# Performance work log

Measured on AMD Instinct MI355X. Metric: run time of the kernel, lower is better.

The kernel has to match this reference:

```python
import jax, jax.numpy as jnp
import numpy as np

# Matches MMD_loss(bandwidths=[1,2,5,10,20])
BANDWIDTHS = np.array([1.0, 2.0, 5.0, 10.0, 20.0], dtype=np.float64)
GAMMAS = (1.0 / (2.0 * BANDWIDTHS ** 2)).astype(np.float32)  # per original forward

N1, N2, D = 4096, 4096, 256


def setup_inputs() -> dict:
    key = jax.random.key(0)
    k1, k2 = jax.random.split(key)
    x1 = jax.random.normal(k1, (N1, D), dtype=jnp.float32)
    x2 = jax.random.normal(k2, (N2, D), dtype=jnp.float32)
    return {"x1": x1, "x2": x2}


def _sqdist(a, b):
    # ||a_i - b_j||^2 via GEMM identity; computed ONCE instead of per-bandwidth.
    an = jnp.sum(a * a, axis=1)  # [Na]
    bn = jnp.sum(b * b, axis=1)  # [Nb]
    d = an[:, None] + bn[None, :] - 2.0 * (a @ b.T)  # [Na, Nb]
    return jnp.maximum(d, 0.0)


def reference(x1, x2):
    d1 = x1.shape[1]
    d2 = x2.shape[1]
    s1 = jnp.float32(np.sqrt(d1))
    s2 = jnp.float32(np.sqrt(d2))

    D11 = _sqdist(x1, x1)  # [N1, N1]
    D22 = _sqdist(x2, x2)  # [N2, N2]
    D12 = _sqdist(x1, x2)  # [N1, N2]

    nb = jnp.float32(len(GAMMAS))
    m11 = jnp.float32(0.0)
    m22 = jnp.float32(0.0)
    m12 = jnp.float32(0.0)
    # small fixed loop over bandwidths; fused exp + mean per bandwidth
    for g in GAMMAS:
        g = jnp.float32(g)
        m11 = m11 + jnp.mean(jnp.exp(-(s1 * g) * D11))
        m22 = m22 + jnp.mean(jnp.exp(-(s2 * g) * D22))
        m12 = m12 + jnp.mean(jnp.exp(-(s1 * g) * D12))  # original uses d1 here too
    m11, m22, m12 = m11 / nb, m22 / nb, m12 / nb
    return jnp.sqrt(m11 - 2.0 * m12 + m22)
```

## Files before the change

kernel.cpp:

```cpp
#include <hip/hip_runtime.h>
#include <stdint.h>

typedef __attribute__((ext_vector_type(8))) short short8;
typedef __attribute__((ext_vector_type(4))) float f32x4;

#define N_ROWS 4096
#define D_DIM  256
#define NT     8192
#define TILE   128
#define NTILE  64

__device__ __forceinline__ unsigned short f2bf(float f) {
  unsigned int u = __float_as_uint(f);
  u += 0x7fffu + ((u >> 16) & 1u);
  return (unsigned short)(u >> 16);
}

__device__ __forceinline__ void gload_lds16(const void* g, void* l) {
  __builtin_amdgcn_global_load_lds(
      (const __attribute__((address_space(1))) unsigned int*)g,
      (__attribute__((address_space(3))) unsigned int*)l, 16, 0, 0);
}

__global__ __launch_bounds__(256) void mmd_prep(
    const float* __restrict__ x1, const float* __restrict__ x2,
    unsigned short* __restrict__ Zb, float* __restrict__ norms) {
  const int t = threadIdx.x, w = t >> 6, l = t & 63;
  const int r = blockIdx.x * 4 + w;
  const float* src = (r < N_ROWS) ? (x1 + (size_t)r * D_DIM)
                                  : (x2 + (size_t)(r - N_ROWS) * D_DIM);
  const float4 v = *(const float4*)(src + l * 4);
  float sq = v.x * v.x + v.y * v.y + v.z * v.z + v.w * v.w;
#pragma unroll
  for (int off = 32; off > 0; off >>= 1) sq += __shfl_down(sq, off);
  if (l == 0) norms[r] = sq;
  ushort4 o;
  o.x = f2bf(v.x); o.y = f2bf(v.y); o.z = f2bf(v.z); o.w = f2bf(v.w);
  *(ushort4*)(Zb + (size_t)r * D_DIM + l * 4) = o;
}

__global__ __launch_bounds__(256) void mmd_main(
    const unsigned short* __restrict__ Zb,
    const float* __restrict__ norms,
    float* __restrict__ partials) {
  const int br = blockIdx.x, bc = blockIdx.y;
  const int pidx = br * NTILE + bc;
  const int t = threadIdx.x;
  if (bc > br) { if (t == 0) partials[pidx] = 0.0f; return; }

  __shared__ __align__(16) unsigned short As[TILE][32];
  __shared__ __align__(16) unsigned short Bs[TILE][32];
  __shared__ float nrow[TILE], ncol[TILE];
  __shared__ float red[256];

  const int w = t >> 6, l = t & 63;
  if (t < TILE) nrow[t] = norms[br * TILE + t];
  else          ncol[t - TILE] = norms[bc * TILE + (t - TILE)];

  const int wr = (w >> 1) * 64, wc = (w & 1) * 64;
  const int fr = l & 15, fq = l >> 4;

  f32x4 acc[4][4];
#pragma unroll
  for (int m = 0; m < 4; ++m)
#pragma unroll
    for (int n = 0; n < 4; ++n)
      acc[m][n] = (f32x4){0.0f, 0.0f, 0.0f, 0.0f};

  for (int k0 = 0; k0 < D_DIM; k0 += 32) {
#pragma unroll
    for (int q = 0; q < 2; ++q) {
      const int obase = w * 2048 + q * 1024;
      const int o = obase + l * 16;
      const int row = o >> 6;
      const int chunk = (o >> 4) & 3;
      const unsigned short* ga =
          Zb + (size_t)(br * TILE + row) * D_DIM + k0 + chunk * 8;
      const unsigned short* gb =
          Zb + (size_t)(bc * TILE + row) * D_DIM + k0 + chunk * 8;
      gload_lds16(ga, (char*)(&As[0][0]) + obase);
      gload_lds16(gb, (char*)(&Bs[0][0]) + obase);
    }
    __syncthreads();

    short8 a[4], b[4];
#pragma unroll
    for (int m = 0; m < 4; ++m)
      a[m] = *(const short8*)(&As[wr + m * 16 + fr][fq * 8]);
#pragma unroll
    for (int n = 0; n < 4; ++n)
      b[n] = *(const short8*)(&Bs[wc + n * 16 + fr][fq * 8]);
#pragma unroll
    for (int m = 0; m < 4; ++m)
#pragma unroll
      for (int n = 0; n < 4; ++n)
        acc[m][n] = __builtin_amdgcn_mfma_f32_16x16x32_bf16(a[m], b[n],
                                                            acc[m][n], 0, 0, 0);
    __syncthreads();
  }

  float factor = ((br < 32) == (bc < 32)) ? 1.0f : -1.0f;
  if (br != bc) factor *= 2.0f;
  const bool diag = (br == bc);

  float sum = 0.0f;
#pragma unroll
  for (int m = 0; m < 4; ++m) {
#pragma unroll
    for (int n = 0; n < 4; ++n) {
#pragma unroll
      for (int r = 0; r < 4; ++r) {
        const int i = wr + m * 16 + fq * 4 + r;
        const int j = wc + n * 16 + fr;
        float d = nrow[i] + ncol[j] - 2.0f * acc[m][n][r];
        d = fmaxf(d, 0.0f);
        const float u = __expf(-0.02f * d);
        const float u2 = u * u, u4 = u2 * u2;
        const float u8 = u4 * u4, u16 = u8 * u8;
        const float u32v = u16 * u16, u64v = u32v * u32v;
        const float u100 = u64v * u32v * u4;
        const float u200 = u100 * u100, u400 = u200 * u200;
        float S = u + u4 + u16 + u100 + u400;
        if (diag && i == j) S = 0.0f;
        sum += S;
      }
    }
  }
  sum *= factor;

  red[t] = sum;
  __syncthreads();
#pragma unroll
  for (int k = 128; k > 0; k >>= 1) {
    if (t < k) red[t] += red[t + k];
    __syncthreads();
  }
  if (t == 0) partials[pidx] = red[0];
}

__global__ __launch_bounds__(256) void mmd_finish(
    const float* __restrict__ partials, float* __restrict__ out) {
  __shared__ float red[256];
  const int t = threadIdx.x;
  float s = 0.0f;
  for (int i = t; i < NTILE * NTILE; i += 256) s += partials[i];
  red[t] = s;
  __syncthreads();
#pragma unroll
  for (int k = 128; k > 0; k >>= 1) {
    if (t < k) red[t] += red[t + k];
    __syncthreads();
  }
  if (t == 0) {
    const float total = red[0] + 40960.0f;
    out[0] = sqrtf(fmaxf(total, 0.0f) / 83886080.0f);
  }
}

extern "C" void kernel_launch(void* const* d_in, const int* in_sizes, int n_in,
                              void* d_out, int out_size, void* d_ws, size_t ws_size,
                              hipStream_t stream) {
  const float* x1 = (const float*)d_in[0];
  const float* x2 = (const float*)d_in[1];
  unsigned short* Zb = (unsigned short*)d_ws;
  float* norms = (float*)((char*)d_ws + (size_t)NT * D_DIM * 2);
  float* partials = norms + NT;
  float* out = (float*)d_out;

  mmd_prep<<<dim3(NT / 4), dim3(256), 0, stream>>>(x1, x2, Zb, norms);
  mmd_main<<<dim3(NTILE, NTILE), dim3(256), 0, stream>>>(Zb, norms, partials);
  mmd_finish<<<dim3(1), dim3(256), 0, stream>>>(partials, out);
}
```

Before: 61.29 us.

## Double-buffer K=64 tiles with swizzled LDS, triangular grid, fuse final reduction

The main kernel now launches only the lower-triangular tile blocks instead of a full 64x64 grid with early exits. The K loop uses 64-wide chunks held in double-buffered LDS, with an XOR swizzle to avoid bank conflicts, so the next chunk is prefetched while the current one computes. Norms are loaded straight into registers rather than staged through shared memory. The separate finish kernel is removed: the last block to finish, found through an atomic counter reset in the prep kernel, does the final reduction. This saves a launch and removes idle blocks, at the cost of more LDS per block (about 65KB) and possibly lower occupancy.

```diff
diff --git a/kernel.cpp b/kernel.cpp
--- a/kernel.cpp
+++ b/kernel.cpp
@@ -8,7 +8,9 @@
 #define D_DIM  256
 #define NT     8192
 #define TILE   128
+#define BK     64
 #define NTILE  64
+#define NBLK   (NTILE * (NTILE + 1) / 2)
 
 __device__ __forceinline__ unsigned short f2bf(float f) {
   unsigned int u = __float_as_uint(f);
@@ -24,7 +26,9 @@
 
 __global__ __launch_bounds__(256) void mmd_prep(
     const float* __restrict__ x1, const float* __restrict__ x2,
-    unsigned short* __restrict__ Zb, float* __restrict__ norms) {
+    unsigned short* __restrict__ Zb, float* __restrict__ norms,
+    unsigned int* __restrict__ counter) {
+  if (blockIdx.x == 0 && threadIdx.x == 0) *counter = 0u;
   const int t = threadIdx.x, w = t >> 6, l = t & 63;
   const int r = blockIdx.x * 4 + w;
   const float* src = (r < N_ROWS) ? (x1 + (size_t)r * D_DIM)
@@ -39,27 +43,43 @@
   *(ushort4*)(Zb + (size_t)r * D_DIM + l * 4) = o;
 }
 
-__global__ __launch_bounds__(256) void mmd_main(
+__global__ __launch_bounds__(256, 2) void mmd_main(
     const unsigned short* __restrict__ Zb,
     const float* __restrict__ norms,
-    float* __restrict__ partials) {
-  const int br = blockIdx.x, bc = blockIdx.y;
-  const int pidx = br * NTILE + bc;
+    float* partials, unsigned int* counter, float* out) {
+  __shared__ __align__(16) unsigned short As[2][TILE * BK];
+  __shared__ __align__(16) unsigned short Bs[2][TILE * BK];
+  __shared__ float red[256];
+  __shared__ int amLastSh;
+
+  const int p = blockIdx.x;
+  int br = (int)((sqrtf(8.0f * (float)p + 1.0f) - 1.0f) * 0.5f);
+  while ((br + 1) * (br + 2) / 2 <= p) ++br;
+  while (br * (br + 1) / 2 > p) --br;
+  const int bc = p - br * (br + 1) / 2;
+
   const int t = threadIdx.x;
-  if (bc > br) { if (t == 0) partials[pidx] = 0.0f; return; }
-
-  __shared__ __align__(16) unsigned short As[TILE][32];
-  __shared__ __align__(16) unsigned short Bs[TILE][32];
-  __shared__ float nrow[TILE], ncol[TILE];
-  __shared__ float red[256];
-
   const int w = t >> 6, l = t & 63;
-  if (t < TILE) nrow[t] = norms[br * TILE + t];
-  else          ncol[t - TILE] = norms[bc * TILE + (t - TILE)];
-
   const int wr = (w >> 1) * 64, wc = (w & 1) * 64;
   const int fr = l & 15, fq = l >> 4;
 
+  const int aRow0 = br * TILE, bRow0 = bc * TILE;
+
+  const int srow = w * 8 + (l >> 3);
+  const int clA = (l & 7) ^ (srow & 7);
+
+#define STAGE(buf, kt)                                                       \
+  do {                                                                       \
+    _Pragma("unroll") for (int q = 0; q < 4; ++q) {                          \
+      const unsigned short* ga = Zb +                                        \
+          (size_t)(aRow0 + q * 32 + srow) * D_DIM + (kt) * BK + clA * 8;     \
+      gload_lds16(ga, (char*)&As[buf][0] + q * 4096 + w * 1024);             \
+      const unsigned short* gb = Zb +                                        \
+          (size_t)(bRow0 + q * 32 + srow) * D_DIM + (kt) * BK + clA * 8;     \
+      gload_lds16(gb, (char*)&Bs[buf][0] + q * 4096 + w * 1024);             \
+    }                                                                        \
+  } while (0)
+
   f32x4 acc[4][4];
 #pragma unroll
   for (int m = 0; m < 4; ++m)
@@ -67,37 +87,52 @@
     for (int n = 0; n < 4; ++n)
       acc[m][n] = (f32x4){0.0f, 0.0f, 0.0f, 0.0f};
 
-  for (int k0 = 0; k0 < D_DIM; k0 += 32) {
-#pragma unroll
-    for (int q = 0; q < 2; ++q) {
-      const int obase = w * 2048 + q * 1024;
-      const int o = obase + l * 16;
-      const int row = o >> 6;
-      const int chunk = (o >> 4) & 3;
-      const unsigned short* ga =
-          Zb + (size_t)(br * TILE + row) * D_DIM + k0 + chunk * 8;
-      const unsigned short* gb =
-          Zb + (size_t)(bc * TILE + row) * D_DIM + k0 + chunk * 8;
-      gload_lds16(ga, (char*)(&As[0][0]) + obase);
-      gload_lds16(gb, (char*)(&Bs[0][0]) + obase);
-    }
+  float nr[16];
+#pragma unroll
+  for (int m = 0; m < 4; ++m)
+#pragma unroll
+    for (int r = 0; r < 4; ++r)
+      nr[m * 4 + r] = norms[aRow0 + wr + m * 16 + fq * 4 + r];
+  float nc[4];
+#pragma unroll
+  for (int n = 0; n < 4; ++n)
+    nc[n] = norms[bRow0 + wc + n * 16 + fr];
+
+#define COMPUTE(buf)                                                         \
+  do {                                                                       \
+    short8 a[4][2], b[4][2];                                                 \
+    _Pragma("unroll") for (int m = 0; m < 4; ++m) {                          \
+      const int row = wr + m * 16 + fr;                                      \
+      _Pragma("unroll") for (int kk = 0; kk < 2; ++kk) {                     \
+        const int cl2 = kk * 4 + fq;                                         \
+        a[m][kk] = *(const short8*)(                                         \
+            &As[buf][row * BK + ((cl2 ^ (row & 7)) << 3)]);                  \
+      }                                                                      \
+    }                                                                        \
+    _Pragma("unroll") for (int n = 0; n < 4; ++n) {                          \
+      const int row = wc + n * 16 + fr;                                      \
+      _Pragma("unroll") for (int kk = 0; kk < 2; ++kk) {                     \
+        const int cl2 = kk * 4 + fq;                                         \
+        b[n][kk] = *(const short8*)(                                         \
+            &Bs[buf][row * BK + ((cl2 ^ (row & 7)) << 3)]);                  \
+      }                                                                      \
+    }                                                                        \
+    _Pragma("unroll") for (int kk = 0; kk < 2; ++kk)                         \
+      _Pragma("unroll") for (int m = 0; m < 4; ++m)                          \
+        _Pragma("unroll") for (int n = 0; n < 4; ++n)                        \
+          acc[m][n] = __builtin_amdgcn_mfma_f32_16x16x32_bf16(               \
+              a[m][kk], b[n][kk], acc[m][n], 0, 0, 0);                       \
+  } while (0)
+
+  STAGE(0, 0);
+  __syncthreads();
+#pragma unroll
+  for (int kt = 0; kt < 3; ++kt) {
+    STAGE((kt + 1) & 1, kt + 1);
+    COMPUTE(kt & 1);
     __syncthreads();
-
-    short8 a[4], b[4];
-#pragma unroll
-    for (int m = 0; m < 4; ++m)
-      a[m] = *(const short8*)(&As[wr + m * 16 + fr][fq * 8]);
-#pragma unroll
-    for (int n = 0; n < 4; ++n)
-      b[n] = *(const short8*)(&Bs[wc + n * 16 + fr][fq * 8]);
-#pragma unroll
-    for (int m = 0; m < 4; ++m)
-#pragma unroll
-      for (int n = 0; n < 4; ++n)
-        acc[m][n] = __builtin_amdgcn_mfma_f32_16x16x32_bf16(a[m], b[n],
-                                                            acc[m][n], 0, 0, 0);
-    __syncthreads();
-  }
+  }
+  COMPUTE(1);
 
   float factor = ((br < 32) == (bc < 32)) ? 1.0f : -1.0f;
   if (br != bc) factor *= 2.0f;
@@ -112,7 +147,7 @@
       for (int r = 0; r < 4; ++r) {
         const int i = wr + m * 16 + fq * 4 + r;
         const int j = wc + n * 16 + fr;
-        float d = nrow[i] + ncol[j] - 2.0f * acc[m][n][r];
+        float d = nr[m * 4 + r] + nc[n] - 2.0f * acc[m][n][r];
         d = fmaxf(d, 0.0f);
         const float u = __expf(-0.02f * d);
         const float u2 = u * u, u4 = u2 * u2;
@@ -135,25 +170,31 @@
     if (t < k) red[t] += red[t + k];
     __syncthreads();
   }
-  if (t == 0) partials[pidx] = red[0];
-}
-
-__global__ __launch_bounds__(256) void mmd_finish(
-    const float* __restrict__ partials, float* __restrict__ out) {
-  __shared__ float red[256];
-  const int t = threadIdx.x;
-  float s = 0.0f;
-  for (int i = t; i < NTILE * NTILE; i += 256) s += partials[i];
-  red[t] = s;
+
+  if (t == 0) {
+    __hip_atomic_store(&partials[p], red[0], __ATOMIC_RELEASE,
+                       __HIP_MEMORY_SCOPE_AGENT);
+    unsigned int old = __hip_atomic_fetch_add(counter, 1u, __ATOMIC_ACQ_REL,
+                                              __HIP_MEMORY_SCOPE_AGENT);
+    amLastSh = (old == NBLK - 1) ? 1 : 0;
+  }
   __syncthreads();
-#pragma unroll
-  for (int k = 128; k > 0; k >>= 1) {
-    if (t < k) red[t] += red[t + k];
+  if (amLastSh) {
+    float s = 0.0f;
+    for (int i = t; i < NBLK; i += 256)
+      s += __hip_atomic_load(&partials[i], __ATOMIC_RELAXED,
+                             __HIP_MEMORY_SCOPE_AGENT);
+    red[t] = s;
     __syncthreads();
-  }
-  if (t == 0) {
-    const float total = red[0] + 40960.0f;
-    out[0] = sqrtf(fmaxf(total, 0.0f) / 83886080.0f);
+#pragma unroll
+    for (int k = 128; k > 0; k >>= 1) {
+      if (t < k) red[t] += red[t + k];
+      __syncthreads();
+    }
+    if (t == 0) {
+      const float total = red[0] + 40960.0f;
+      out[0] = sqrtf(fmaxf(total, 0.0f) / 83886080.0f);
+    }
   }
 }
 
@@ -165,9 +206,9 @@
   unsigned short* Zb = (unsigned short*)d_ws;
   float* norms = (float*)((char*)d_ws + (size_t)NT * D_DIM * 2);
   float* partials = norms + NT;
+  unsigned int* counter = (unsigned int*)(partials + NBLK);
   float* out = (float*)d_out;
 
-  mmd_prep<<<dim3(NT / 4), dim3(256), 0, stream>>>(x1, x2, Zb, norms);
-  mmd_main<<<dim3(NTILE, NTILE), dim3(256), 0, stream>>>(Zb, norms, partials);
-  mmd_finish<<<dim3(1), dim3(256), 0, stream>>>(partials, out);
-}
+  mmd_prep<<<dim3(NT / 4), dim3(256), 0, stream>>>(x1, x2, Zb, norms, counter);
+  mmd_main<<<dim3(NBLK), dim3(256), 0, stream>>>(Zb, norms, partials, counter, out);
+}
```

Result: slower. 94.08 us (+53.5%).
